# Performance work log

Hardware: AMD Instinct MI355X
Metric: run time of the kernel (lower is better)

Reference implementation:

```python
import jax, jax.numpy as jnp
import numpy as np

DIM = 1024
HEADS = 16
HEAD_DIM = DIM // HEADS
SCALE = HEAD_DIM ** -0.5


def setup_inputs() -> dict:
    key = jax.random.key(0)
    ks = jax.random.split(key, 6)
    B, N, C = 2, 2048, DIM
    s = C ** -0.5
    return {
        "x": jax.random.normal(ks[0], (B, N, C), dtype=jnp.float32),
        "Wq": jax.random.normal(ks[1], (C, C), dtype=jnp.float32) * s,
        "Wk": jax.random.normal(ks[2], (C, C), dtype=jnp.float32) * s,
        "Wv": jax.random.normal(ks[3], (C, C), dtype=jnp.float32) * s,
        "Wo": jax.random.normal(ks[4], (C, C), dtype=jnp.float32) * s,
        "bo": jax.random.normal(ks[5], (C,), dtype=jnp.float32) * 0.02,
    }


def reference(x, Wq, Wk, Wv, Wo, bo):
    B, N, C = x.shape
    H, D = HEADS, HEAD_DIM
    # q/k/v linears (no bias), reshape to [B, H, N, D]
    q = (x @ Wq.T).reshape(B, N, H, D).transpose(0, 2, 1, 3)
    k = (x @ Wk.T).reshape(B, N, H, D).transpose(0, 2, 1, 3)
    v = (x @ Wv.T).reshape(B, N, H, D).transpose(0, 2, 1, 3)
    attn = jnp.einsum("bhnd,bhmd->bhnm", q, k) * SCALE  # [B,H,N,N]
    attn = jax.nn.softmax(attn, axis=-1)
    out = jnp.einsum("bhnm,bhmd->bhnd", attn, v)  # [B,H,N,D]
    out = out.transpose(0, 2, 1, 3).reshape(B, N, C)
    out = out @ Wo.T + bo  # proj (dropout p=0 in eval -> identity)
    return out
```

## Files before the change

kernel.cpp:

```cpp
#include <hip/hip_runtime.h>
#include <stdint.h>

typedef __attribute__((ext_vector_type(8))) _Float16 half8;
typedef __attribute__((ext_vector_type(8))) unsigned short ushort8;
typedef __attribute__((ext_vector_type(4))) float f32x4;
typedef unsigned short u16;

#define AS1C(p) ((const __attribute__((address_space(1))) void*)(p))
#define AS3(p)  ((__attribute__((address_space(3))) void*)(p))

#define PIPE_WAIT(n) do { asm volatile("s_waitcnt vmcnt(" #n ")" ::: "memory"); \
  __builtin_amdgcn_s_barrier(); __builtin_amdgcn_sched_barrier(0); } while (0)

__device__ __forceinline__ f32x4 mfma_k32(half8 a, half8 b, f32x4 c) {
  return __builtin_amdgcn_mfma_f32_16x16x32_f16(a, b, c, 0, 0, 0);
}
__device__ __forceinline__ u16 f2h(float f) {
  return __builtin_bit_cast(u16, (_Float16)f);
}
__device__ __forceinline__ float fexp2(float x) {
  return __builtin_amdgcn_exp2f(x);
}
__device__ __forceinline__ unsigned int pk2h(float a, float b) {
  return __builtin_bit_cast(unsigned int, __builtin_amdgcn_cvt_pkrtz(a, b));
}
__device__ __forceinline__ int fsz(int r) {
  return (((r & 3) | (((r >> 3) & 1) << 2)) << 4);
}

__global__ __launch_bounds__(256) void k_convert(
    const float* __restrict__ x, const float* __restrict__ wq,
    const float* __restrict__ wk, const float* __restrict__ wv,
    const float* __restrict__ wo,
    u16* __restrict__ xb, u16* __restrict__ wqkvb, u16* __restrict__ wob) {
  size_t t = (size_t)blockIdx.x * 256 + threadIdx.x;
  size_t e = t * 8;
  const float* src;
  u16* dst;
  if (e < 4194304u)      { src = x  + e;            dst = xb    + e; }
  else if (e < 5242880u) { src = wq + (e-4194304u); dst = wqkvb + (e-4194304u); }
  else if (e < 6291456u) { src = wk + (e-5242880u); dst = wqkvb + (e-4194304u); }
  else if (e < 7340032u) { src = wv + (e-6291456u); dst = wqkvb + (e-4194304u); }
  else                   { src = wo + (e-7340032u); dst = wob   + (e-7340032u); }
  float4 a = *(const float4*)src;
  float4 b = *(const float4*)(src + 4);
  ushort8 o;
  o[0]=f2h(a.x); o[1]=f2h(a.y); o[2]=f2h(a.z); o[3]=f2h(a.w);
  o[4]=f2h(b.x); o[5]=f2h(b.y); o[6]=f2h(b.z); o[7]=f2h(b.w);
  *(ushort8*)dst = o;
}

__global__ __launch_bounds__(512) void k_gemm_qkv(
    const u16* __restrict__ xb, const u16* __restrict__ wqkvb,
    u16* __restrict__ qk, u16* __restrict__ vt) {
  __shared__ u16 lA[3 * 4096];
  __shared__ u16 lB[3 * 4096];
  char* lAc = (char*)lA;
  char* lBc = (char*)lB;
  const int lid = blockIdx.x;
  const int xcd = lid & 7, idx = lid >> 3;
  const int pr = idx / 12, pc = idx % 12;
  const int row0 = (((xcd & 3) << 3) + pr) << 7;
  const int col0 = ((xcd >> 2) * 12 + pc) << 7;

  const int tid = threadIdx.x;
  const int w = tid >> 6, lane = tid & 63;
  const int wm = (w & 1) * 64, wn = (w >> 1) * 32;
  const int l15 = lane & 15, l4 = lane >> 4;
  f32x4 acc[4][2];
#pragma unroll
  for (int i = 0; i < 4; ++i)
#pragma unroll
    for (int j = 0; j < 2; ++j) acc[i][j] = (f32x4){0.f, 0.f, 0.f, 0.f};

  const int lrow = lane >> 2;
  const int lcb  = (lane & 3) << 4;
  const char* Abase = (const char*)xb + (size_t)row0 * 2048;
  const char* Bbase = (const char*)wqkvb + (size_t)col0 * 2048;

  auto stage = [&](int buf, int kt) {
    int r = (w << 4) + lrow;
    __builtin_amdgcn_global_load_lds(AS1C(Abase + (size_t)r * 2048 + kt * 64 + lcb),
                                     AS3(lAc + buf * 8192 + w * 1024), 16, 0, 0);
    __builtin_amdgcn_global_load_lds(AS1C(Bbase + (size_t)r * 2048 + kt * 64 + lcb),
                                     AS3(lBc + buf * 8192 + w * 1024), 16, 0, 0);
  };
  auto compute = [&](int buf) {
    const char* A = lAc + buf * 8192;
    const char* B = lBc + buf * 8192;
    half8 af[4], bf[2];
#pragma unroll
    for (int mi = 0; mi < 4; ++mi)
      af[mi] = *(const half8*)(A + (wm + mi * 16 + l15) * 64 + (l4 << 4));
#pragma unroll
    for (int ni = 0; ni < 2; ++ni)
      bf[ni] = *(const half8*)(B + (wn + ni * 16 + l15) * 64 + (l4 << 4));
#pragma unroll
    for (int mi = 0; mi < 4; ++mi)
#pragma unroll
      for (int ni = 0; ni < 2; ++ni)
        acc[mi][ni] = mfma_k32(af[mi], bf[ni], acc[mi][ni]);
  };

  stage(0, 0);
  stage(1, 1);
  for (int k3 = 0; k3 < 30; k3 += 3) {
    PIPE_WAIT(2); stage(2, k3 + 2); compute(0);
    PIPE_WAIT(2); stage(0, k3 + 3); compute(1);
    PIPE_WAIT(2); stage(1, k3 + 4); compute(2);
  }
  PIPE_WAIT(2); compute(0);
  PIPE_WAIT(0); compute(1);

  const int rbase = row0 + wm + (l4 << 2);
  const int cbase = col0 + wn + l15;
  const bool isQ = (col0 < 1024);
  const bool isV = (col0 >= 2048);
#pragma unroll
  for (int mi = 0; mi < 4; ++mi) {
#pragma unroll
    for (int ni = 0; ni < 2; ++ni) {
      const int col = cbase + ni * 16;
      if (!isV) {
#pragma unroll
        for (int r = 0; r < 4; ++r) {
          int row = rbase + mi * 16 + r;
          float v = acc[mi][ni][r];
          if (isQ) v *= 0.18033688f;
          qk[(size_t)row * 2048 + col] = f2h(v);
        }
      } else {
        const int jj = col - 2048;
        const int h = jj >> 6, d = jj & 63;
        const int row = rbase + mi * 16;
        const int b = row >> 11, n = row & 2047;
        u16 pk[4];
#pragma unroll
        for (int r = 0; r < 4; ++r) pk[r] = f2h(acc[mi][ni][r]);
        *(uint2*)&vt[(size_t)(((b << 4) + h) * 64 + d) * 2048 + n] = *(uint2*)pk;
      }
    }
  }
}

__global__ __launch_bounds__(512) void k_attn(
    const u16* __restrict__ qk, const u16* __restrict__ vt, u16* __restrict__ ao) {
  __shared__ u16 KV[6][4096];
  char* L = (char*)&KV[0][0];
  const int lid = blockIdx.x;
  const int xcd = lid & 7, sub = lid >> 3;
  const int bh = (xcd << 2) + (sub >> 4);
  const int qt = sub & 15;
  const int b = bh >> 4, h = bh & 15;
  const int w = threadIdx.x >> 6, lane = threadIdx.x & 63;
  const int l15 = lane & 15, l4 = lane >> 4;

  const int qrow = (b << 11) + (qt << 7) + (w << 4) + l15;
  half8 qf[2];
  qf[0] = *(const half8*)(qk + (size_t)qrow * 2048 + h * 64 + (l4 << 3));
  qf[1] = *(const half8*)(qk + (size_t)qrow * 2048 + h * 64 + 32 + (l4 << 3));

  half8 vones8;
#pragma unroll
  for (int j = 0; j < 8; ++j) vones8[j] = (_Float16)1.0f;

  const int lrow = lane >> 3;
  const int lcb  = (lane & 7) << 4;
  const char* Kbase = (const char*)qk + (size_t)(b << 11) * 4096 + 2048 + h * 128;
  const char* Vbase = (const char*)vt + (size_t)(bh * 64) * 4096;

  const int rr0 = (w << 3) + lrow;
  const int sc0 = lcb ^ fsz(rr0);
  const char* kg0 = Kbase + (size_t)rr0 * 4096 + sc0;
  const char* vg0 = Vbase + (size_t)rr0 * 4096 + sc0;
  const int kd0 = w * 1024;

  const int keybase = ((l15 >> 2) << 3) + (l15 & 3);
  const int kswz = fsz(keybase);
  const int vswz = (((l15 & 3) | (((l15 >> 3) & 1) << 2)) << 4);
  int koff[8], voff[8];
#pragma unroll
  for (int nt = 0; nt < 4; ++nt) {
    const int key = keybase + ((nt & 1) << 2) + ((nt >> 1) << 5);
    koff[2 * nt]     = key * 128 + ((l4 << 4) ^ kswz);
    koff[2 * nt + 1] = key * 128 + (((l4 << 4) + 64) ^ kswz);
  }
#pragma unroll
  for (int dt = 0; dt < 4; ++dt) {
    const int d = dt * 16 + l15;
    voff[2 * dt]     = 24576 + d * 128 + ((l4 << 4) ^ vswz);
    voff[2 * dt + 1] = 24576 + d * 128 + (((l4 << 4) + 64) ^ vswz);
  }

  float m_run = -1e30f;
  f32x4 acc_o[4];
  f32x4 acc_l = (f32x4){0.f, 0.f, 0.f, 0.f};
#pragma unroll
  for (int dt = 0; dt < 4; ++dt) acc_o[dt] = (f32x4){0.f, 0.f, 0.f, 0.f};

  auto stage = [&](int buf) {
    __builtin_amdgcn_global_load_lds(AS1C(kg0), AS3(L + buf * 8192 + kd0), 16, 0, 0);
    __builtin_amdgcn_global_load_lds(AS1C(vg0), AS3(L + 24576 + buf * 8192 + kd0), 16, 0, 0);
    kg0 += 262144; vg0 += 128;
  };

  auto compute = [&](int bu) {
    const char* Lb = L + bu * 8192;

    f32x4 s[4];
    __builtin_amdgcn_s_setprio(1);
#pragma unroll
    for (int nt = 0; nt < 4; ++nt) {
      half8 k0 = *(const half8*)(Lb + koff[2 * nt]);
      half8 k1 = *(const half8*)(Lb + koff[2 * nt + 1]);
      f32x4 z = (f32x4){0.f, 0.f, 0.f, 0.f};
      z = mfma_k32(k0, qf[0], z);
      s[nt] = mfma_k32(k1, qf[1], z);
    }
    __builtin_amdgcn_s_setprio(0);

    float t0 = fmaxf(fmaxf(s[0][0], s[0][1]), s[0][2]);
    float t1 = fmaxf(fmaxf(s[0][3], s[1][0]), s[1][1]);
    float t2 = fmaxf(fmaxf(s[1][2], s[1][3]), s[2][0]);
    float t3 = fmaxf(fmaxf(s[2][1], s[2][2]), s[2][3]);
    float t4 = fmaxf(fmaxf(s[3][0], s[3][1]), s[3][2]);
    float tm = fmaxf(fmaxf(fmaxf(t0, t1), fmaxf(t2, t3)), fmaxf(t4, s[3][3]));

    const bool skip = __all(tm - m_run <= 8.f);
    float mnew = m_run;
    if (!skip) {
      tm = fmaxf(tm, __shfl_xor(tm, 16));
      tm = fmaxf(tm, __shfl_xor(tm, 32));
      mnew = fmaxf(m_run, tm);
      float alpha = fexp2(m_run - mnew);
      m_run = mnew;
#pragma unroll
      for (int dt = 0; dt < 4; ++dt)
#pragma unroll
        for (int r = 0; r < 4; ++r) acc_o[dt][r] *= alpha;
      acc_l[0] *= alpha;
    }

    half8 pb[2];
#pragma unroll
    for (int p = 0; p < 2; ++p) {
      uint4 pk;
      pk.x = pk2h(fexp2(s[2*p][0] - mnew),   fexp2(s[2*p][1] - mnew));
      pk.y = pk2h(fexp2(s[2*p][2] - mnew),   fexp2(s[2*p][3] - mnew));
      pk.z = pk2h(fexp2(s[2*p+1][0] - mnew), fexp2(s[2*p+1][1] - mnew));
      pk.w = pk2h(fexp2(s[2*p+1][2] - mnew), fexp2(s[2*p+1][3] - mnew));
      pb[p] = __builtin_bit_cast(half8, pk);
    }

    __builtin_amdgcn_s_setprio(1);
#pragma unroll
    for (int dt = 0; dt < 4; ++dt) {
      half8 v0 = *(const half8*)(Lb + voff[2 * dt]);
      half8 v1 = *(const half8*)(Lb + voff[2 * dt + 1]);
      acc_o[dt] = mfma_k32(v0, pb[0], acc_o[dt]);
      acc_o[dt] = mfma_k32(v1, pb[1], acc_o[dt]);
    }
    acc_l = mfma_k32(vones8, pb[0], acc_l);
    acc_l = mfma_k32(vones8, pb[1], acc_l);
    __builtin_amdgcn_s_setprio(0);
  };

  stage(0);
  stage(1);
  for (int k3 = 0; k3 < 30; k3 += 3) {
    PIPE_WAIT(2); stage(2); compute(0);
    PIPE_WAIT(2); stage(0); compute(1);
    PIPE_WAIT(2); stage(1); compute(2);
  }
  PIPE_WAIT(2); compute(0);
  PIPE_WAIT(0); compute(1);

  const float inv = __builtin_amdgcn_rcpf(acc_l[0]);
  const size_t rowbase = ((size_t)(b << 11) + (qt << 7) + (w << 4) + l15) * 1024 + h * 64;
#pragma unroll
  for (int dt = 0; dt < 4; ++dt) {
    uint2 o;
    o.x = pk2h(acc_o[dt][0] * inv, acc_o[dt][1] * inv);
    o.y = pk2h(acc_o[dt][2] * inv, acc_o[dt][3] * inv);
    *(uint2*)&ao[rowbase + dt * 16 + (l4 << 2)] = o;
  }
}

__global__ __launch_bounds__(256) void k_gemm_proj(
    const u16* __restrict__ aob, const u16* __restrict__ wob,
    const float* __restrict__ bo, float* __restrict__ out) {
  __shared__ u16 lA[3 * 4096];
  __shared__ u16 lB[3 * 2048];
  const int lid = blockIdx.x;
  const int xcd = lid & 7, idx = lid >> 3;
  const int row0 = ((xcd << 2) + (idx >> 4)) << 7;
  const int col0 = (idx & 15) << 6;

  const int tid = threadIdx.x;
  const int w = tid >> 6, lane = tid & 63;
  const int wm = (w >> 1) * 64, wn = (w & 1) * 32;
  const int l15 = lane & 15, l4 = lane >> 4;
  f32x4 acc[4][2];
#pragma unroll
  for (int i = 0; i < 4; ++i)
#pragma unroll
    for (int j = 0; j < 2; ++j) acc[i][j] = (f32x4){0.f, 0.f, 0.f, 0.f};

  const int lrow = lane >> 2;
  const int lcb  = (lane & 3) << 4;
  const char* Abase = (const char*)aob + (size_t)row0 * 2048;
  const char* Bbase = (const char*)wob + (size_t)col0 * 2048;
  char* lAc = (char*)lA;
  char* lBc = (char*)lB;

  auto stage = [&](int buf, int kt) {
#pragma unroll
    for (int i = 0; i < 2; ++i) {
      int c = w + 4 * i;
      int r = c * 16 + lrow;
      __builtin_amdgcn_global_load_lds(AS1C(Abase + (size_t)r * 2048 + kt * 64 + lcb),
                                       AS3(lAc + buf * 8192 + c * 1024), 16, 0, 0);
    }
    int rb = w * 16 + lrow;
    __builtin_amdgcn_global_load_lds(AS1C(Bbase + (size_t)rb * 2048 + kt * 64 + lcb),
                                     AS3(lBc + buf * 4096 + w * 1024), 16, 0, 0);
  };
  auto compute = [&](int buf) {
    const char* A = lAc + buf * 8192;
    const char* B = lBc + buf * 4096;
    half8 af[4], bf[2];
#pragma unroll
    for (int mi = 0; mi < 4; ++mi)
      af[mi] = *(const half8*)(A + (wm + mi * 16 + l15) * 64 + (l4 << 4));
#pragma unroll
    for (int ni = 0; ni < 2; ++ni)
      bf[ni] = *(const half8*)(B + (wn + ni * 16 + l15) * 64 + (l4 << 4));
#pragma unroll
    for (int mi = 0; mi < 4; ++mi)
#pragma unroll
      for (int ni = 0; ni < 2; ++ni)
        acc[mi][ni] = mfma_k32(af[mi], bf[ni], acc[mi][ni]);
  };

  stage(0, 0);
  stage(1, 1);
  for (int k3 = 0; k3 < 30; k3 += 3) {
    PIPE_WAIT(3); stage(2, k3 + 2); compute(0);
    PIPE_WAIT(3); stage(0, k3 + 3); compute(1);
    PIPE_WAIT(3); stage(1, k3 + 4); compute(2);
  }
  PIPE_WAIT(3); compute(0);
  PIPE_WAIT(0); compute(1);

  const int rbase = row0 + wm + (l4 << 2);
  const int cbase = col0 + wn + l15;
#pragma unroll
  for (int mi = 0; mi < 4; ++mi) {
#pragma unroll
    for (int ni = 0; ni < 2; ++ni) {
      const int col = cbase + ni * 16;
      const float bb = bo[col];
#pragma unroll
      for (int r = 0; r < 4; ++r) {
        const int row = rbase + mi * 16 + r;
        out[(size_t)row * 1024 + col] = acc[mi][ni][r] + bb;
      }
    }
  }
}

extern "C" void kernel_launch(void* const* d_in, const int* in_sizes, int n_in,
                              void* d_out, int out_size, void* d_ws, size_t ws_size,
                              hipStream_t stream) {
  const float* x  = (const float*)d_in[0];
  const float* wq = (const float*)d_in[1];
  const float* wk = (const float*)d_in[2];
  const float* wv = (const float*)d_in[3];
  const float* wo = (const float*)d_in[4];
  const float* bo = (const float*)d_in[5];
  float* out = (float*)d_out;

  char* ws = (char*)d_ws;
  u16* xb    = (u16*)(ws);
  u16* wqkvb = (u16*)(ws + 8388608);
  u16* wob   = (u16*)(ws + 14680064);
  u16* qkb   = (u16*)(ws + 16777216);
  u16* vtb   = (u16*)(ws + 33554432);
  u16* aob   = (u16*)(ws + 41943040);

  k_convert<<<dim3(4096), dim3(256), 0, stream>>>(x, wq, wk, wv, wo, xb, wqkvb, wob);
  k_gemm_qkv<<<dim3(768), dim3(512), 0, stream>>>(xb, wqkvb, qkb, vtb);
  k_attn<<<dim3(512), dim3(512), 0, stream>>>(qkb, vtb, aob);
  k_gemm_proj<<<dim3(512), dim3(256), 0, stream>>>(aob, wob, bo, out);
}
```

Before: 111.9 us.

## Split attention over key range into two halves and combine with log-sum-exp

```diff
diff --git a/kernel.cpp b/kernel.cpp
--- a/kernel.cpp
+++ b/kernel.cpp
@@ -144,13 +144,16 @@
 }
 
 __global__ __launch_bounds__(512) void k_attn(
-    const u16* __restrict__ qk, const u16* __restrict__ vt, u16* __restrict__ ao) {
+    const u16* __restrict__ qk, const u16* __restrict__ vt,
+    u16* __restrict__ po, float* __restrict__ se) {
   __shared__ u16 KV[6][4096];
   char* L = (char*)&KV[0][0];
   const int lid = blockIdx.x;
   const int xcd = lid & 7, sub = lid >> 3;
-  const int bh = (xcd << 2) + (sub >> 4);
-  const int qt = sub & 15;
+  const int bh = (xcd << 2) + (sub >> 5);
+  const int r5 = sub & 31;
+  const int qt = r5 >> 1;
+  const int split = r5 & 1;
   const int b = bh >> 4, h = bh & 15;
   const int w = threadIdx.x >> 6, lane = threadIdx.x & 63;
   const int l15 = lane & 15, l4 = lane >> 4;
@@ -171,8 +174,8 @@
 
   const int rr0 = (w << 3) + lrow;
   const int sc0 = lcb ^ fsz(rr0);
-  const char* kg0 = Kbase + (size_t)rr0 * 4096 + sc0;
-  const char* vg0 = Vbase + (size_t)rr0 * 4096 + sc0;
+  const char* kg0 = Kbase + (size_t)rr0 * 4096 + sc0 + (size_t)split * 4194304;
+  const char* vg0 = Vbase + (size_t)rr0 * 4096 + sc0 + split * 2048;
   const int kd0 = w * 1024;
 
   const int keybase = ((l15 >> 2) << 3) + (l15 & 3);
@@ -267,23 +270,54 @@
 
   stage(0);
   stage(1);
-  for (int k3 = 0; k3 < 30; k3 += 3) {
+  for (int k3 = 0; k3 < 12; k3 += 3) {
     PIPE_WAIT(2); stage(2); compute(0);
     PIPE_WAIT(2); stage(0); compute(1);
     PIPE_WAIT(2); stage(1); compute(2);
   }
-  PIPE_WAIT(2); compute(0);
-  PIPE_WAIT(0); compute(1);
+  PIPE_WAIT(2); stage(2); compute(0);
+  PIPE_WAIT(2); stage(0); compute(1);
+  PIPE_WAIT(2); compute(2);
+  PIPE_WAIT(0); compute(0);
 
   const float inv = __builtin_amdgcn_rcpf(acc_l[0]);
+  u16* po_s = po + (size_t)split * 4194304;
   const size_t rowbase = ((size_t)(b << 11) + (qt << 7) + (w << 4) + l15) * 1024 + h * 64;
 #pragma unroll
   for (int dt = 0; dt < 4; ++dt) {
     uint2 o;
     o.x = pk2h(acc_o[dt][0] * inv, acc_o[dt][1] * inv);
     o.y = pk2h(acc_o[dt][2] * inv, acc_o[dt][3] * inv);
-    *(uint2*)&ao[rowbase + dt * 16 + (l4 << 2)] = o;
-  }
+    *(uint2*)&po_s[rowbase + dt * 16 + (l4 << 2)] = o;
+  }
+  if (l4 == 0) {
+    float sv = m_run + __log2f(acc_l[0]);
+    se[(size_t)split * 65536 + bh * 2048 + (qt << 7) + (w << 4) + l15] = sv;
+  }
+}
+
+__global__ __launch_bounds__(256) void k_comb(
+    u16* __restrict__ po, const float* __restrict__ se) {
+  size_t t = (size_t)blockIdx.x * 256 + threadIdx.x;
+  size_t e = t * 8;
+  const int row = (int)(e >> 10);
+  const int col = (int)(e & 1023);
+  const int h = col >> 6;
+  const int b = row >> 11, n = row & 2047;
+  const int bh = (b << 4) + h;
+  const float s0 = se[bh * 2048 + n];
+  const float s1 = se[65536 + bh * 2048 + n];
+  const float sm = fmaxf(s0, s1);
+  float w0 = fexp2(s0 - sm), w1 = fexp2(s1 - sm);
+  const float inv = 1.f / (w0 + w1);
+  w0 *= inv; w1 *= inv;
+  half8 o0 = *(const half8*)(po + e);
+  half8 o1 = *(const half8*)(po + 4194304 + e);
+  ushort8 o;
+#pragma unroll
+  for (int j = 0; j < 8; ++j)
+    o[j] = f2h(w0 * (float)o0[j] + w1 * (float)o1[j]);
+  *(ushort8*)(po + e) = o;
 }
 
 __global__ __launch_bounds__(256) void k_gemm_proj(
@@ -386,10 +420,12 @@
   u16* wob   = (u16*)(ws + 14680064);
   u16* qkb   = (u16*)(ws + 16777216);
   u16* vtb   = (u16*)(ws + 33554432);
-  u16* aob   = (u16*)(ws + 41943040);
+  u16* pob   = (u16*)(ws + 41943040);
+  float* seb = (float*)(ws + 58720256);
 
   k_convert<<<dim3(4096), dim3(256), 0, stream>>>(x, wq, wk, wv, wo, xb, wqkvb, wob);
   k_gemm_qkv<<<dim3(768), dim3(512), 0, stream>>>(xb, wqkvb, qkb, vtb);
-  k_attn<<<dim3(512), dim3(512), 0, stream>>>(qkb, vtb, aob);
-  k_gemm_proj<<<dim3(512), dim3(256), 0, stream>>>(aob, wob, bo, out);
-}
+  k_attn<<<dim3(1024), dim3(512), 0, stream>>>(qkb, vtb, pob, seb);
+  k_comb<<<dim3(2048), dim3(256), 0, stream>>>(pob, seb);
+  k_gemm_proj<<<dim3(512), dim3(256), 0, stream>>>(pob, wob, bo, out);
+}
```

After: 119.3 us. 1.07x slower.
